# Kernel tuning notes

Hardware: AMD Instinct MI355X
Metric: run time of the kernel (lower is better)

The kernel has to match this reference:

```python
import jax, jax.numpy as jnp
import numpy as np

N, IN, HID, OUT, HEADS, E = 50000, 256, 128, 128, 2, 800000
NEG_SLOPE = 0.2


def gat_conv(x, edge_src, edge_dst, W, att_src, att_dst, bias):
    # x: [N, F_in]; W: [F_in, H*C]; att_*: [H, C]; bias: [C]
    n = x.shape[0]
    H, C = att_src.shape
    xl = (x @ W).reshape(n, H, C)                       # [N, H, C]
    a_src = jnp.sum(xl * att_src, axis=-1)              # [N, H]
    a_dst = jnp.sum(xl * att_dst, axis=-1)              # [N, H]
    e = jax.nn.leaky_relu(a_src[edge_src] + a_dst[edge_dst], NEG_SLOPE)  # [E+N, H]
    e_max = jax.ops.segment_max(e, edge_dst, num_segments=n)            # [N, H]
    e = jnp.exp(e - e_max[edge_dst])
    denom = jax.ops.segment_sum(e, edge_dst, num_segments=n)            # [N, H]
    alpha = e / (denom[edge_dst] + 1e-16)                               # [E+N, H]
    msg = xl[edge_src] * alpha[:, :, None]                              # [E+N, H, C]
    out = jax.ops.segment_sum(msg, edge_dst, num_segments=n)            # [N, H, C]
    return out.mean(axis=1) + bias                                      # concat=False: head mean


def setup_inputs() -> dict:
    key = jax.random.key(0)
    ks = jax.random.split(key, 12)
    x = jax.random.normal(ks[0], (N, IN), dtype=jnp.float32)
    edge_index = jax.random.randint(ks[1], (2, E), 0, N, dtype=jnp.int64)
    s = 0.1
    W0 = jax.random.normal(ks[2], (IN, HEADS * HID), dtype=jnp.float32) * s
    att_src0 = jax.random.normal(ks[3], (HEADS, HID), dtype=jnp.float32) * s
    att_dst0 = jax.random.normal(ks[4], (HEADS, HID), dtype=jnp.float32) * s
    bias0 = jnp.zeros((HID,), dtype=jnp.float32)
    W1 = jax.random.normal(ks[5], (HID, HEADS * HID), dtype=jnp.float32) * s
    att_src1 = jax.random.normal(ks[6], (HEADS, HID), dtype=jnp.float32) * s
    att_dst1 = jax.random.normal(ks[7], (HEADS, HID), dtype=jnp.float32) * s
    bias1 = jnp.zeros((HID,), dtype=jnp.float32)
    proj_w = jax.random.normal(ks[8], (HID, OUT), dtype=jnp.float32) * s
    proj_b = jnp.zeros((OUT,), dtype=jnp.float32)
    return {"x": x, "edge_index": edge_index,
            "W0": W0, "att_src0": att_src0, "att_dst0": att_dst0, "bias0": bias0,
            "W1": W1, "att_src1": att_src1, "att_dst1": att_dst1, "bias1": bias1,
            "proj_w": proj_w, "proj_b": proj_b}


def reference(x, edge_index, W0, att_src0, att_dst0, bias0, W1, att_src1, att_dst1, bias1, proj_w, proj_b):
    n = x.shape[0]
    loops = jnp.arange(n, dtype=edge_index.dtype)
    # PyG GATConv default add_self_loops=True
    src = jnp.concatenate([edge_index[0], loops])
    dst = jnp.concatenate([edge_index[1], loops])
    h = gat_conv(x, src, dst, W0, att_src0, att_dst0, bias0)
    h = jax.nn.gelu(h, approximate=False)
    h = gat_conv(h, src, dst, W1, att_src1, att_dst1, bias1)
    h = jax.nn.gelu(h, approximate=False)
    return h @ proj_w + proj_b
```

## Files before the change

kernel.cpp:

```cpp
#include <hip/hip_runtime.h>
#include <hip/hip_fp16.h>
#include <math.h>


#define NEG_SLOPE 0.2f

typedef __attribute__((ext_vector_type(8))) _Float16 f16x8;
typedef __attribute__((ext_vector_type(8))) ushort u16x8;
typedef __attribute__((ext_vector_type(4))) float f32x4;

__device__ __forceinline__ ushort f32_to_f16u(float x)
{
    return __half_as_ushort(__float2half(x));
}

__device__ __forceinline__ float f16u_to_f32(ushort u)
{
    return __half2float(__ushort_as_half(u));
}

__device__ __forceinline__ void split_f16(float x, ushort& h, ushort& l)
{
    const __half hh = __float2half(x);
    h = __half_as_ushort(hh);
    l = __half_as_ushort(__float2half(x - __half2float(hh)));
}

__device__ __forceinline__ float lrelu(float x)
{
    return x > 0.f ? x : NEG_SLOPE * x;
}

__device__ __forceinline__ float gelu_exact(float x)
{
    return 0.5f * x * (1.0f + erff(x * 0.7071067811865476f));
}

__global__ __launch_bounds__(256)
void prep_kernel(const float* __restrict__ W0, const float* __restrict__ W1,
                 const float* __restrict__ PW,
                 const float* __restrict__ as0, const float* __restrict__ ad0,
                 const float* __restrict__ as1, const float* __restrict__ ad1,
                 ushort* __restrict__ w0h, ushort* __restrict__ w0l,
                 ushort* __restrict__ w1h, ushort* __restrict__ w1l,
                 ushort* __restrict__ pwh, ushort* __restrict__ pwl,
                 float* __restrict__ wtd0, float* __restrict__ wt1,
                 int* __restrict__ cnt, int N)
{
    const int blk = blockIdx.x;
    if (blk >= 577) {
        int t2 = (blk - 577) * 256 + threadIdx.x;
        if (t2 < N) cnt[t2] = 0;
        return;
    }
    if (blk == 576) {
        const int col = threadIdx.x;
        float4 o;
        if (col < 128) o = make_float4(as0[col], 0.f, ad0[col], 0.f);
        else           o = make_float4(0.f, as0[col], 0.f, ad0[col]);
        *(float4*)(wtd0 + col * 4) = o;
        return;
    }
    if (blk < 448) {
        int t = blk * 256 + threadIdx.x;
        ushort h, l;
        if (t < 65536) {
            int k = t >> 8, n = t & 255;
            split_f16(W0[t], h, l);
            w0h[n * 256 + k] = h; w0l[n * 256 + k] = l;
        } else if (t < 65536 + 32768) {
            int u = t - 65536;
            int k = u >> 8, n = u & 255;
            split_f16(W1[u], h, l);
            w1h[n * 128 + k] = h; w1l[n * 128 + k] = l;
        } else {
            int u = t - 65536 - 32768;
            int k = u >> 7, n = u & 127;
            split_f16(PW[u], h, l);
            pwh[n * 128 + k] = h; pwl[n * 128 + k] = l;
        }
        return;
    }
    const int k = blk - 448;
    const int t = threadIdx.x;
    const int h = t >> 7, c = t & 127;
    const int lane = t & 63, wid = t >> 6;
    const float w = W1[(size_t)k * 256 + h * 128 + c];
    float ps = w * as1[h * 128 + c];
    float pd = w * ad1[h * 128 + c];
#pragma unroll
    for (int off = 1; off < 64; off <<= 1) {
        ps += __shfl_xor(ps, off, 64);
        pd += __shfl_xor(pd, off, 64);
    }
    __shared__ float sm[4][2];
    if (lane == 0) { sm[wid][0] = ps; sm[wid][1] = pd; }
    __syncthreads();
    if (t == 0) {
        wt1[k * 4 + 0] = sm[0][0] + sm[1][0];
        wt1[k * 4 + 1] = sm[2][0] + sm[3][0];
        wt1[k * 4 + 2] = sm[0][1] + sm[1][1];
        wt1[k * 4 + 3] = sm[2][1] + sm[3][1];
    }
}

template<int BN, bool SPLITA>
__global__ __launch_bounds__(512)
void mfma_gemm3(const float* __restrict__ Af,
                const ushort* __restrict__ A16,
                const ushort* __restrict__ Bth, const ushort* __restrict__ Btl,
                const float* __restrict__ bias,
                float* __restrict__ Cf, ushort* __restrict__ Cb,
                const float* __restrict__ watt,
                float* __restrict__ a_sc, float* __restrict__ a_dc,
                int M, int K)
{
    constexpr int NF = BN / 64;
    __shared__ ushort Ah[4][128][8];
    __shared__ ushort Bh[4][BN][8];
    __shared__ ushort Bl[4][BN][8];

    const int tid = threadIdx.x;
    const int r0 = blockIdx.x * 128;
    const int w = tid >> 6, lane = tid & 63;
    const int wr = (w & 1) * 64;
    const int wc = (w >> 1) * (BN / 4);
    const int lr = lane & 15, kb = lane >> 4;

    const int arow = tid >> 2;
    const int apl = tid & 3;

    f32x4 acc[4][NF] = {};

    for (int kk = 0; kk < K; kk += 32) {
        {
            const int row = r0 + arow;
            u16x8 h0 = {};
            if (row < M) {
                if constexpr (SPLITA) {
                    const float* p = Af + (size_t)row * K + kk + apl * 8;
                    float4 v0 = *(const float4*)(p);
                    float4 v1 = *(const float4*)(p + 4);
                    h0[0] = f32_to_f16u(v0.x); h0[1] = f32_to_f16u(v0.y);
                    h0[2] = f32_to_f16u(v0.z); h0[3] = f32_to_f16u(v0.w);
                    h0[4] = f32_to_f16u(v1.x); h0[5] = f32_to_f16u(v1.y);
                    h0[6] = f32_to_f16u(v1.z); h0[7] = f32_to_f16u(v1.w);
                } else {
                    h0 = *(const u16x8*)(A16 + (size_t)row * K + kk + apl * 8);
                }
            }
            *(u16x8*)&Ah[apl][arow][0] = h0;
        }
        if constexpr (BN == 256) {
            const int col = tid >> 1, half = tid & 1;
            const ushort* ph = Bth + (size_t)col * K + kk + half * 16;
            const ushort* pl = Btl + (size_t)col * K + kk + half * 16;
            *(u16x8*)&Bh[half * 2 + 0][col][0] = *(const u16x8*)(ph);
            *(u16x8*)&Bh[half * 2 + 1][col][0] = *(const u16x8*)(ph + 8);
            *(u16x8*)&Bl[half * 2 + 0][col][0] = *(const u16x8*)(pl);
            *(u16x8*)&Bl[half * 2 + 1][col][0] = *(const u16x8*)(pl + 8);
        } else {
            const int col = tid >> 2, pl = tid & 3;
            *(u16x8*)&Bh[pl][col][0] = *(const u16x8*)(Bth + (size_t)col * K + kk + pl * 8);
            *(u16x8*)&Bl[pl][col][0] = *(const u16x8*)(Btl + (size_t)col * K + kk + pl * 8);
        }
        __syncthreads();

        f16x8 ah[4];
#pragma unroll
        for (int m = 0; m < 4; ++m)
            ah[m] = *(const f16x8*)&Ah[kb][wr + m * 16 + lr][0];
#pragma unroll
        for (int n = 0; n < NF; ++n) {
            const f16x8 bh = *(const f16x8*)&Bh[kb][wc + n * 16 + lr][0];
            const f16x8 bl = *(const f16x8*)&Bl[kb][wc + n * 16 + lr][0];
#pragma unroll
            for (int m = 0; m < 4; ++m) {
                acc[m][n] = __builtin_amdgcn_mfma_f32_16x16x32_f16(ah[m], bh, acc[m][n], 0, 0, 0);
                acc[m][n] = __builtin_amdgcn_mfma_f32_16x16x32_f16(ah[m], bl, acc[m][n], 0, 0, 0);
            }
        }
        __syncthreads();
    }

#pragma unroll
    for (int n = 0; n < NF; ++n) {
        const int col = wc + n * 16 + lr;
        const float bv = bias ? bias[col] : 0.f;
#pragma unroll
        for (int m = 0; m < 4; ++m) {
            const int rowb = r0 + wr + m * 16 + kb * 4;
#pragma unroll
            for (int j = 0; j < 4; ++j) {
                const int row = rowb + j;
                if (row < M) {
                    const float val = acc[m][n][j] + bv;
                    if (Cf) Cf[(size_t)row * BN + col] = val;
                    if (Cb) Cb[(size_t)row * BN + col] = f32_to_f16u(val);
                }
            }
        }
    }

    if (watt) {
        float* sp = (float*)&Ah[0][0][0];
        float4 wv[NF];
#pragma unroll
        for (int n = 0; n < NF; ++n)
            wv[n] = *(const float4*)(watt + (wc + n * 16 + lr) * 4);
#pragma unroll
        for (int m = 0; m < 4; ++m) {
#pragma unroll
            for (int j = 0; j < 4; ++j) {
                float s0 = 0.f, s1 = 0.f, s2 = 0.f, s3 = 0.f;
#pragma unroll
                for (int n = 0; n < NF; ++n) {
                    const float v = acc[m][n][j];
                    s0 += v * wv[n].x;
                    s1 += v * wv[n].y;
                    s2 += v * wv[n].z;
                    s3 += v * wv[n].w;
                }
#pragma unroll
                for (int off = 1; off < 16; off <<= 1) {
                    s0 += __shfl_xor(s0, off, 64);
                    s1 += __shfl_xor(s1, off, 64);
                    s2 += __shfl_xor(s2, off, 64);
                    s3 += __shfl_xor(s3, off, 64);
                }
                if (lr == 0) {
                    const int row = wr + m * 16 + kb * 4 + j;
                    float* d = sp + ((w >> 1) * 128 + row) * 4;
                    d[0] = s0; d[1] = s1; d[2] = s2; d[3] = s3;
                }
            }
        }
        __syncthreads();
        const int row = tid >> 2, comp = tid & 3;
        const float s = sp[(0 * 128 + row) * 4 + comp]
                      + sp[(1 * 128 + row) * 4 + comp]
                      + sp[(2 * 128 + row) * 4 + comp]
                      + sp[(3 * 128 + row) * 4 + comp];
        const int gr = r0 + row;
        if (gr < M) {
            if (comp < 2) a_sc[(size_t)gr * 2 + comp] = s;
            else          a_dc[(size_t)gr * 2 + (comp - 2)] = s;
        }
    }
}

__global__ __launch_bounds__(256)
void gat_gather_kernel(const ushort* __restrict__ xlb,
                       const int* __restrict__ rowptr,
                       const int* __restrict__ esrc,
                       const float* __restrict__ a_si,
                       const float* __restrict__ a_di,
                       const float* __restrict__ bias,
                       const float* __restrict__ watt,
                       float* __restrict__ a_so, float* __restrict__ a_do,
                       ushort* __restrict__ outh,
                       int n)
{
    const int wave = threadIdx.x >> 6;
    const int lane = threadIdx.x & 63;
    const int v = blockIdx.x * 4 + wave;
    if (v >= n) return;
    const int h = lane >> 5;
    const int j0 = lane & 31;
    const int c4 = j0 << 2;

    const float adv = a_di[v * 2 + h];
    const float wself = __expf(lrelu(a_si[v * 2 + h] + adv));

    const ushort4 xv4 = *(const ushort4*)(xlb + (size_t)v * 256 + (lane << 2));
    float4 acc0, acc1;
    acc0.x = wself * f16u_to_f32(xv4.x);
    acc0.y = wself * f16u_to_f32(xv4.y);
    acc0.z = wself * f16u_to_f32(xv4.z);
    acc0.w = wself * f16u_to_f32(xv4.w);
    acc1 = make_float4(0.f, 0.f, 0.f, 0.f);
    float ssum = (j0 == 0) ? wself : 0.f;

    const int beg = rowptr[v], end = rowptr[v + 1];
    for (int i = beg; i < end; i += 32) {
        const int cnt = min(32, end - i);
        int myidx = 0;
        float myw = 0.f;
        if (j0 < cnt) {
            myidx = esrc[i + j0];
            myw = __expf(lrelu(a_si[myidx * 2 + h] + adv));
        }
        ssum += myw;
#pragma unroll 2
        for (int j = 0; j < cnt; ++j) {
            const int src = __builtin_amdgcn_readlane(myidx, j);
            const float wgt = __shfl(myw, j, 32);
            const ushort4 xs4 = *(const ushort4*)(xlb + (size_t)src * 256 + (lane << 2));
            if (j & 1) {
                acc1.x += wgt * f16u_to_f32(xs4.x);
                acc1.y += wgt * f16u_to_f32(xs4.y);
                acc1.z += wgt * f16u_to_f32(xs4.z);
                acc1.w += wgt * f16u_to_f32(xs4.w);
            } else {
                acc0.x += wgt * f16u_to_f32(xs4.x);
                acc0.y += wgt * f16u_to_f32(xs4.y);
                acc0.z += wgt * f16u_to_f32(xs4.z);
                acc0.w += wgt * f16u_to_f32(xs4.w);
            }
        }
    }

#pragma unroll
    for (int off = 1; off < 32; off <<= 1)
        ssum += __shfl_xor(ssum, off, 64);
    const float inv = 1.0f / (ssum + 1e-16f);

    float4 r;
    r.x = (acc0.x + acc1.x) * inv;
    r.y = (acc0.y + acc1.y) * inv;
    r.z = (acc0.z + acc1.z) * inv;
    r.w = (acc0.w + acc1.w) * inv;
    float4 o;
    o.x = 0.5f * (r.x + __shfl_xor(r.x, 32, 64));
    o.y = 0.5f * (r.y + __shfl_xor(r.y, 32, 64));
    o.z = 0.5f * (r.z + __shfl_xor(r.z, 32, 64));
    o.w = 0.5f * (r.w + __shfl_xor(r.w, 32, 64));

    const float4 bb = *(const float4*)(bias + c4);
    o.x = gelu_exact(o.x + bb.x);
    o.y = gelu_exact(o.y + bb.y);
    o.z = gelu_exact(o.z + bb.z);
    o.w = gelu_exact(o.w + bb.w);

    if (watt) {
        const float ov[4] = {o.x, o.y, o.z, o.w};
        float s0 = 0.f, s1 = 0.f, d0 = 0.f, d1 = 0.f;
#pragma unroll
        for (int i = 0; i < 4; ++i) {
            const float4 wv = *(const float4*)(watt + (c4 + i) * 4);
            s0 += ov[i] * wv.x;
            s1 += ov[i] * wv.y;
            d0 += ov[i] * wv.z;
            d1 += ov[i] * wv.w;
        }
#pragma unroll
        for (int off = 1; off < 64; off <<= 1) {
            s0 += __shfl_xor(s0, off, 64);
            s1 += __shfl_xor(s1, off, 64);
            d0 += __shfl_xor(d0, off, 64);
            d1 += __shfl_xor(d1, off, 64);
        }
        if (lane == 0) {
            *(float2*)(a_so + (size_t)v * 2) = make_float2(0.5f * s0, 0.5f * s1);
            *(float2*)(a_do + (size_t)v * 2) = make_float2(0.5f * d0, 0.5f * d1);
        }
    }

    if (lane < 32) {
        ushort4 st;
        st.x = f32_to_f16u(o.x);
        st.y = f32_to_f16u(o.y);
        st.z = f32_to_f16u(o.z);
        st.w = f32_to_f16u(o.w);
        *(ushort4*)(outh + (size_t)v * 128 + c4) = st;
    }
}

__global__ __launch_bounds__(256)
void hist_kernel(const int* __restrict__ ei, int* __restrict__ cnt, int E)
{
    int e = blockIdx.x * 256 + threadIdx.x;
    if (e < E) atomicAdd(&cnt[ei[E + e]], 1);
}

__global__ __launch_bounds__(256)
void blocksum_kernel(const int* __restrict__ cnt, int* __restrict__ bsum, int n)
{
    __shared__ int sm[256];
    const int t = threadIdx.x;
    const int i = blockIdx.x * 256 + t;
    sm[t] = (i < n) ? cnt[i] : 0;
    __syncthreads();
#pragma unroll
    for (int off = 1; off < 256; off <<= 1) {
        int u = (t >= off) ? sm[t - off] : 0;
        __syncthreads();
        sm[t] += u;
        __syncthreads();
    }
    if (t == 255) bsum[blockIdx.x] = sm[255];
}

__global__ __launch_bounds__(256)
void scan_bsum_kernel(int* __restrict__ bsum, int nb, int* __restrict__ ptr, int n)
{
    __shared__ int sm[256];
    const int t = threadIdx.x;
    const int v = (t < nb) ? bsum[t] : 0;
    sm[t] = v;
    __syncthreads();
#pragma unroll
    for (int off = 1; off < 256; off <<= 1) {
        int u = (t >= off) ? sm[t - off] : 0;
        __syncthreads();
        sm[t] += u;
        __syncthreads();
    }
    if (t < nb) bsum[t] = sm[t] - v;
    if (t == 255) ptr[n] = sm[255];
}

__global__ __launch_bounds__(256)
void scan_out_kernel(const int* __restrict__ cnt, const int* __restrict__ bsum,
                     int* __restrict__ ptr, int* __restrict__ pcur, int n)
{
    __shared__ int sm[256];
    const int t = threadIdx.x;
    const int i = blockIdx.x * 256 + t;
    const int v = (i < n) ? cnt[i] : 0;
    sm[t] = v;
    __syncthreads();
#pragma unroll
    for (int off = 1; off < 256; off <<= 1) {
        int u = (t >= off) ? sm[t - off] : 0;
        __syncthreads();
        sm[t] += u;
        __syncthreads();
    }
    if (i < n) {
        const int val = bsum[blockIdx.x] + sm[t] - v;
        ptr[i] = val;
        pcur[i] = val;
    }
}

__global__ __launch_bounds__(256)
void scatter_kernel(const int* __restrict__ ei, int* __restrict__ pcur,
                    int* __restrict__ esrc, int E)
{
    int e = blockIdx.x * 256 + threadIdx.x;
    if (e < E) {
        int dst = ei[E + e];
        int src = ei[e];
        int pos = atomicAdd(&pcur[dst], 1);
        esrc[pos] = src;
    }
}

extern "C" void kernel_launch(void* const* d_in, const int* in_sizes, int n_in,
                              void* d_out, int out_size, void* d_ws, size_t ws_size,
                              hipStream_t stream)
{
    const float* x       = (const float*)d_in[0];
    const int*   ei      = (const int*)d_in[1];
    const float* W0      = (const float*)d_in[2];
    const float* att_s0  = (const float*)d_in[3];
    const float* att_d0  = (const float*)d_in[4];
    const float* b0      = (const float*)d_in[5];
    const float* W1      = (const float*)d_in[6];
    const float* att_s1  = (const float*)d_in[7];
    const float* att_d1  = (const float*)d_in[8];
    const float* b1      = (const float*)d_in[9];
    const float* pw      = (const float*)d_in[10];
    const float* pb      = (const float*)d_in[11];

    const int N = in_sizes[0] / 256;
    const int E = in_sizes[1] / 2;
    const int NB = (N + 255) / 256;

    ushort* xlb  = (ushort*)d_ws;
    ushort* hbuf = xlb + (size_t)N * 256;
    float*  a_s  = (float*)(hbuf + (size_t)N * 128);
    float*  a_d  = a_s + (size_t)N * 2;
    float*  a_s2 = a_d + (size_t)N * 2;
    float*  a_d2 = a_s2 + (size_t)N * 2;
    float*  wtd0 = a_d2 + (size_t)N * 2;
    float*  wt1  = wtd0 + 256 * 4;
    int*    cnt  = (int*)(wt1 + 128 * 4);
    int*    ptr  = cnt + N;
    int*    pcur = ptr + (N + 1);
    int*    bsm  = pcur + N;
    int*    esr  = bsm + 256;
    ushort* w0h  = (ushort*)(esr + E);
    ushort* w0l  = w0h + 256 * 256;
    ushort* w1h  = w0l + 256 * 256;
    ushort* w1l  = w1h + 256 * 128;
    ushort* pwh  = w1l + 256 * 128;
    ushort* pwl  = pwh + 128 * 128;

    const int ablk = (N + 3) / 4;
    const int eblk = (E + 255) / 256;
    const int gblk = (N + 127) / 128;

    prep_kernel<<<577 + NB, 256, 0, stream>>>(
        W0, W1, pw, att_s0, att_d0, att_s1, att_d1,
        w0h, w0l, w1h, w1l, pwh, pwl, wtd0, wt1, cnt, N);

    hist_kernel<<<eblk, 256, 0, stream>>>(ei, cnt, E);
    blocksum_kernel<<<NB, 256, 0, stream>>>(cnt, bsm, N);
    scan_bsum_kernel<<<1, 256, 0, stream>>>(bsm, NB, ptr, N);
    scan_out_kernel<<<NB, 256, 0, stream>>>(cnt, bsm, ptr, pcur, N);
    scatter_kernel<<<eblk, 256, 0, stream>>>(ei, pcur, esr, E);

    mfma_gemm3<256, true><<<gblk, 512, 0, stream>>>(
        x, nullptr, w0h, w0l, nullptr, nullptr, xlb, wtd0, a_s, a_d, N, 256);
    gat_gather_kernel<<<ablk, 256, 0, stream>>>(
        xlb, ptr, esr, a_s, a_d, b0, wt1, a_s2, a_d2, hbuf, N);

    mfma_gemm3<256, false><<<gblk, 512, 0, stream>>>(
        nullptr, hbuf, w1h, w1l, nullptr, nullptr, xlb, nullptr, nullptr, nullptr, N, 128);
    gat_gather_kernel<<<ablk, 256, 0, stream>>>(
        xlb, ptr, esr, a_s2, a_d2, b1, nullptr, nullptr, nullptr, hbuf, N);

    mfma_gemm3<128, false><<<gblk, 512, 0, stream>>>(
        nullptr, hbuf, pwh, pwl, pb, (float*)d_out, nullptr, nullptr, nullptr, nullptr, N, 128);
}
```

Baseline: 332.1 us.

## Split wave into two half-waves gathering different edges with 16-byte loads

Result: faster. 325.6 us (median of 2 runs) (-2.0%).

```diff
diff --git a/kernel.cpp b/kernel.cpp
--- a/kernel.cpp
+++ b/kernel.cpp
@@ -265,104 +265,109 @@
     const int lane = threadIdx.x & 63;
     const int v = blockIdx.x * 4 + wave;
     if (v >= n) return;
-    const int h = lane >> 5;
-    const int j0 = lane & 31;
-    const int c4 = j0 << 2;
-
-    const float adv = a_di[v * 2 + h];
-    const float wself = __expf(lrelu(a_si[v * 2 + h] + adv));
-
-    const ushort4 xv4 = *(const ushort4*)(xlb + (size_t)v * 256 + (lane << 2));
-    float4 acc0, acc1;
-    acc0.x = wself * f16u_to_f32(xv4.x);
-    acc0.y = wself * f16u_to_f32(xv4.y);
-    acc0.z = wself * f16u_to_f32(xv4.z);
-    acc0.w = wself * f16u_to_f32(xv4.w);
-    acc1 = make_float4(0.f, 0.f, 0.f, 0.f);
-    float ssum = (j0 == 0) ? wself : 0.f;
+    const int half = lane >> 5;
+    const int il = lane & 31;
+    const int ch8 = il << 3;
+    const int hsel = il >> 4;
+
+    const float2 advv = *(const float2*)(a_di + (size_t)v * 2);
+    const float2 asvv = *(const float2*)(a_si + (size_t)v * 2);
+    const float wself0 = __expf(lrelu(asvv.x + advv.x));
+    const float wself1 = __expf(lrelu(asvv.y + advv.y));
+    const float wselfh = hsel ? wself1 : wself0;
+
+    const u16x8 xv = *(const u16x8*)(xlb + (size_t)v * 256 + ch8);
+    float acc[8];
+#pragma unroll
+    for (int k = 0; k < 8; ++k)
+        acc[k] = (half == 0) ? wselfh * f16u_to_f32(xv[k]) : 0.f;
+
+    float ssum0 = (il == 0) ? wself0 : 0.f;
+    float ssum1 = (il == 0) ? wself1 : 0.f;
 
     const int beg = rowptr[v], end = rowptr[v + 1];
     for (int i = beg; i < end; i += 32) {
         const int cnt = min(32, end - i);
         int myidx = 0;
-        float myw = 0.f;
-        if (j0 < cnt) {
-            myidx = esrc[i + j0];
-            myw = __expf(lrelu(a_si[myidx * 2 + h] + adv));
-        }
-        ssum += myw;
+        float myw0 = 0.f, myw1 = 0.f;
+        if (il < cnt) {
+            myidx = esrc[i + il];
+            const float2 e = *(const float2*)(a_si + (size_t)myidx * 2);
+            myw0 = __expf(lrelu(e.x + advv.x));
+            myw1 = __expf(lrelu(e.y + advv.y));
+        }
+        ssum0 += myw0;
+        ssum1 += myw1;
 #pragma unroll 2
-        for (int j = 0; j < cnt; ++j) {
-            const int src = __builtin_amdgcn_readlane(myidx, j);
-            const float wgt = __shfl(myw, j, 32);
-            const ushort4 xs4 = *(const ushort4*)(xlb + (size_t)src * 256 + (lane << 2));
-            if (j & 1) {
-                acc1.x += wgt * f16u_to_f32(xs4.x);
-                acc1.y += wgt * f16u_to_f32(xs4.y);
-                acc1.z += wgt * f16u_to_f32(xs4.z);
-                acc1.w += wgt * f16u_to_f32(xs4.w);
-            } else {
-                acc0.x += wgt * f16u_to_f32(xs4.x);
-                acc0.y += wgt * f16u_to_f32(xs4.y);
-                acc0.z += wgt * f16u_to_f32(xs4.z);
-                acc0.w += wgt * f16u_to_f32(xs4.w);
-            }
-        }
-    }
-
-#pragma unroll
-    for (int off = 1; off < 32; off <<= 1)
-        ssum += __shfl_xor(ssum, off, 64);
-    const float inv = 1.0f / (ssum + 1e-16f);
-
-    float4 r;
-    r.x = (acc0.x + acc1.x) * inv;
-    r.y = (acc0.y + acc1.y) * inv;
-    r.z = (acc0.z + acc1.z) * inv;
-    r.w = (acc0.w + acc1.w) * inv;
-    float4 o;
-    o.x = 0.5f * (r.x + __shfl_xor(r.x, 32, 64));
-    o.y = 0.5f * (r.y + __shfl_xor(r.y, 32, 64));
-    o.z = 0.5f * (r.z + __shfl_xor(r.z, 32, 64));
-    o.w = 0.5f * (r.w + __shfl_xor(r.w, 32, 64));
-
-    const float4 bb = *(const float4*)(bias + c4);
-    o.x = gelu_exact(o.x + bb.x);
-    o.y = gelu_exact(o.y + bb.y);
-    o.z = gelu_exact(o.z + bb.z);
-    o.w = gelu_exact(o.w + bb.w);
-
-    if (watt) {
-        const float ov[4] = {o.x, o.y, o.z, o.w};
-        float s0 = 0.f, s1 = 0.f, d0 = 0.f, d1 = 0.f;
-#pragma unroll
-        for (int i = 0; i < 4; ++i) {
-            const float4 wv = *(const float4*)(watt + (c4 + i) * 4);
-            s0 += ov[i] * wv.x;
-            s1 += ov[i] * wv.y;
-            d0 += ov[i] * wv.z;
-            d1 += ov[i] * wv.w;
-        }
-#pragma unroll
-        for (int off = 1; off < 64; off <<= 1) {
-            s0 += __shfl_xor(s0, off, 64);
-            s1 += __shfl_xor(s1, off, 64);
-            d0 += __shfl_xor(d0, off, 64);
-            d1 += __shfl_xor(d1, off, 64);
-        }
-        if (lane == 0) {
-            *(float2*)(a_so + (size_t)v * 2) = make_float2(0.5f * s0, 0.5f * s1);
-            *(float2*)(a_do + (size_t)v * 2) = make_float2(0.5f * d0, 0.5f * d1);
-        }
-    }
-
-    if (lane < 32) {
-        ushort4 st;
-        st.x = f32_to_f16u(o.x);
-        st.y = f32_to_f16u(o.y);
-        st.z = f32_to_f16u(o.z);
-        st.w = f32_to_f16u(o.w);
-        *(ushort4*)(outh + (size_t)v * 128 + c4) = st;
+        for (int j = 0; j < cnt; j += 2) {
+            const int jj = j + half;
+            const int src = __shfl(myidx, jj, 32);
+            const float w0 = __shfl(myw0, jj, 32);
+            const float w1 = __shfl(myw1, jj, 32);
+            const float wgt = hsel ? w1 : w0;
+            const u16x8 xs = *(const u16x8*)(xlb + (size_t)src * 256 + ch8);
+#pragma unroll
+            for (int k = 0; k < 8; ++k)
+                acc[k] += wgt * f16u_to_f32(xs[k]);
+        }
+    }
+
+#pragma unroll
+    for (int off = 1; off <= 16; off <<= 1) {
+        ssum0 += __shfl_xor(ssum0, off, 64);
+        ssum1 += __shfl_xor(ssum1, off, 64);
+    }
+    const float inv = 1.0f / ((hsel ? ssum1 : ssum0) + 1e-16f);
+
+    float o[8];
+#pragma unroll
+    for (int k = 0; k < 8; ++k) {
+        float a = acc[k] + __shfl_xor(acc[k], 32, 64);
+        a *= inv;
+        o[k] = 0.5f * (a + __shfl_xor(a, 16, 64));
+    }
+
+    if (il < 16) {
+        const float4 bb0 = *(const float4*)(bias + ch8);
+        const float4 bb1 = *(const float4*)(bias + ch8 + 4);
+        o[0] = gelu_exact(o[0] + bb0.x);
+        o[1] = gelu_exact(o[1] + bb0.y);
+        o[2] = gelu_exact(o[2] + bb0.z);
+        o[3] = gelu_exact(o[3] + bb0.w);
+        o[4] = gelu_exact(o[4] + bb1.x);
+        o[5] = gelu_exact(o[5] + bb1.y);
+        o[6] = gelu_exact(o[6] + bb1.z);
+        o[7] = gelu_exact(o[7] + bb1.w);
+
+        if (watt) {
+            float s0 = 0.f, s1 = 0.f, d0 = 0.f, d1 = 0.f;
+#pragma unroll
+            for (int k = 0; k < 8; ++k) {
+                const float4 wv = *(const float4*)(watt + (ch8 + k) * 4);
+                s0 += o[k] * wv.x;
+                s1 += o[k] * wv.y;
+                d0 += o[k] * wv.z;
+                d1 += o[k] * wv.w;
+            }
+#pragma unroll
+            for (int off = 1; off <= 8; off <<= 1) {
+                s0 += __shfl_xor(s0, off, 64);
+                s1 += __shfl_xor(s1, off, 64);
+                d0 += __shfl_xor(d0, off, 64);
+                d1 += __shfl_xor(d1, off, 64);
+            }
+            if (lane == 0) {
+                *(float2*)(a_so + (size_t)v * 2) = make_float2(s0, s1);
+                *(float2*)(a_do + (size_t)v * 2) = make_float2(d0, d1);
+            }
+        }
+
+        if (half == 0) {
+            u16x8 st;
+#pragma unroll
+            for (int k = 0; k < 8; ++k) st[k] = f32_to_f16u(o[k]);
+            *(u16x8*)(outh + (size_t)v * 128 + ch8) = st;
+        }
     }
 }
 
```
